# Optimization experiments

Hardware: AMD Instinct MI355X
Metric: run time of the kernel (lower is better)

Reference implementation:

```python
import jax, jax.numpy as jnp
import numpy as np
import math

DIM = 1024
N_HEADS = 16
HEAD_DIM = DIM // N_HEADS
FFN_HIDDEN = 4096
EPS = 1e-6


def setup_inputs() -> dict:
    key = jax.random.key(0)
    ks = jax.random.split(key, 10)
    s = 1.0 / math.sqrt(DIM)
    sh = 1.0 / math.sqrt(FFN_HIDDEN)
    return {
        "x": jax.random.normal(ks[0], (2, 2048, DIM), dtype=jnp.float32),
        # attention weights stored as [in, out] (y = x @ W)
        "wq": jax.random.normal(ks[1], (DIM, DIM), dtype=jnp.float32) * s,
        "wk": jax.random.normal(ks[2], (DIM, DIM), dtype=jnp.float32) * s,
        "wv": jax.random.normal(ks[3], (DIM, DIM), dtype=jnp.float32) * s,
        "wo": jax.random.normal(ks[4], (DIM, DIM), dtype=jnp.float32) * s,
        "w_gate": jax.random.normal(ks[5], (DIM, FFN_HIDDEN), dtype=jnp.float32) * s,
        "w_up": jax.random.normal(ks[6], (DIM, FFN_HIDDEN), dtype=jnp.float32) * s,
        "w_down": jax.random.normal(ks[7], (FFN_HIDDEN, DIM), dtype=jnp.float32) * sh,
        "attn_norm_w": jnp.ones((DIM,), dtype=jnp.float32),
        "ffn_norm_w": jnp.ones((DIM,), dtype=jnp.float32),
    }


def rmsnorm(x, w):
    xf = x.astype(jnp.float32)
    rms = jax.lax.rsqrt(jnp.mean(xf * xf, axis=-1, keepdims=True) + EPS)
    return (xf * rms).astype(x.dtype) * w


def attention(x, wq, wk, wv, wo):
    B, T, C = x.shape
    q = (x @ wq).reshape(B, T, N_HEADS, HEAD_DIM)
    k = (x @ wk).reshape(B, T, N_HEADS, HEAD_DIM)
    v = (x @ wv).reshape(B, T, N_HEADS, HEAD_DIM)
    scores = jnp.einsum("bqhd,bkhd->bhqk", q, k) / math.sqrt(HEAD_DIM)
    causal = jnp.tril(jnp.ones((T, T), dtype=bool))  # True = keep
    scores = jnp.where(causal, scores, -jnp.inf)
    attn = jax.nn.softmax(scores, axis=-1)
    out = jnp.einsum("bhqk,bkhd->bqhd", attn, v).reshape(B, T, C)
    return out @ wo


def swiglu(x, w_gate, w_up, w_down):
    return (jax.nn.silu(x @ w_gate) * (x @ w_up)) @ w_down


def reference(x, wq, wk, wv, wo, w_gate, w_up, w_down, attn_norm_w, ffn_norm_w):
    x = x + attention(rmsnorm(x, attn_norm_w), wq, wk, wv, wo)
    x = x + swiglu(rmsnorm(x, ffn_norm_w), w_gate, w_up, w_down)
    return x
```

## Files before the change

### kernel.cpp

```cpp
#include <hip/hip_runtime.h>
#include <hip/hip_bf16.h>
#include <stdint.h>
#include <math.h>

#define DIM   1024
#define TSEQ  2048
#define BATCH 2
#define NH    16
#define HD    64
#define FFN   4096
#define ROWS  (BATCH*TSEQ)
#define QKVN  (3*DIM)

typedef __attribute__((ext_vector_type(8))) short s16x8;
typedef __attribute__((ext_vector_type(4))) float f32x4;

__device__ __forceinline__ unsigned short f2bf(float f) {
  union { float f; unsigned u; } v; v.f = f;
  unsigned r = v.u + 0x7fffu + ((v.u >> 16) & 1u);
  return (unsigned short)(r >> 16);
}
__device__ __forceinline__ float bf2f(unsigned short h) {
  union { unsigned u; float f; } v; v.u = ((unsigned)h) << 16; return v.f;
}
__device__ __forceinline__ unsigned pack_bf2(float lo, float hi) {
  union { float f; unsigned u; } a, c; a.f = lo; c.f = hi;
  return (c.u & 0xffff0000u) | (a.u >> 16);
}

__device__ __forceinline__ void gld16(const void* g, void* l) {
  __builtin_amdgcn_global_load_lds((const __attribute__((address_space(1))) void*)g,
                                   (__attribute__((address_space(3))) void*)l, 16, 0, 0);
}

__device__ __forceinline__ int xcd_swz_flat() {
  const int nx = gridDim.x, ny = gridDim.y;
  const int nwg = nx * ny * gridDim.z;
  const int flat = blockIdx.x + nx * (blockIdx.y + ny * blockIdx.z);
  return (flat & 7) * (nwg >> 3) + (flat >> 3);
}

__global__ void wtrans_k(const float* __restrict__ w, unsigned short* __restrict__ wt,
                         int K, int N, int mode)
{
  __shared__ unsigned short t[64][65];
  const int n0 = blockIdx.x * 64, k0 = blockIdx.y * 64;
  const int tid = threadIdx.x;
  #pragma unroll
  for (int i = 0; i < 16; ++i) {
    const int r = i*4 + (tid >> 6), c = tid & 63;
    t[r][c] = f2bf(w[(size_t)(k0 + r) * N + n0 + c]);
  }
  __syncthreads();
  #pragma unroll
  for (int i = 0; i < 16; ++i) {
    const int r = i*4 + (tid >> 6), c = tid & 63;
    const int n = n0 + r;
    int dr = n;
    if (mode == 1) dr = ((n >> 4) << 5) + (n & 15);
    if (mode == 2) dr = ((n >> 4) << 5) + 16 + (n & 15);
    wt[(size_t)dr * K + k0 + c] = t[c][r];
  }
}

__global__ void wtrans_qkv_k(const float* __restrict__ wq, const float* __restrict__ wk,
                             const float* __restrict__ wv, unsigned short* __restrict__ wt)
{
  __shared__ unsigned short t[64][65];
  const int n0 = blockIdx.x * 64, k0 = blockIdx.y * 64, z = blockIdx.z;
  const float* w = (z == 0) ? wq : (z == 1) ? wk : wv;
  unsigned short* dst = wt + (size_t)z * DIM * DIM;
  const int tid = threadIdx.x;
  #pragma unroll
  for (int i = 0; i < 16; ++i) {
    const int r = i*4 + (tid >> 6), c = tid & 63;
    t[r][c] = f2bf(w[(size_t)(k0 + r) * DIM + n0 + c]);
  }
  __syncthreads();
  #pragma unroll
  for (int i = 0; i < 16; ++i) {
    const int r = i*4 + (tid >> 6), c = tid & 63;
    dst[(size_t)(n0 + r) * DIM + k0 + c] = t[c][r];
  }
}

__global__ void vtrans_k(const unsigned short* __restrict__ qkv, unsigned short* __restrict__ vt)
{
  __shared__ unsigned short t[64][65];
  const int tt0 = blockIdx.x * 64;
  const int bh = blockIdx.y, b = bh >> 4, h = bh & 15;
  const int tid = threadIdx.x;
  const unsigned short* src = qkv + (size_t)(b*TSEQ + tt0) * QKVN + 2*DIM + h*HD;
  #pragma unroll
  for (int i = 0; i < 16; ++i) {
    const int r = i*4 + (tid >> 6), c = tid & 63;
    t[r][c] = src[(size_t)r * QKVN + c];
  }
  __syncthreads();
  unsigned short* dst = vt + (size_t)bh * HD * TSEQ + tt0;
  #pragma unroll
  for (int i = 0; i < 16; ++i) {
    const int d = i*4 + (tid >> 6), c = tid & 63;
    dst[(size_t)d * TSEQ + c] = t[c][d];
  }
}

__global__ void rmsnorm_k(const float* __restrict__ x, const float* __restrict__ w,
                          unsigned short* __restrict__ o)
{
  const int row = blockIdx.x, tid = threadIdx.x;
  const float4 v = ((const float4*)(x + (size_t)row * DIM))[tid];
  float ss = v.x*v.x + v.y*v.y + v.z*v.z + v.w*v.w;
  #pragma unroll
  for (int off = 32; off >= 1; off >>= 1) ss += __shfl_xor(ss, off);
  __shared__ float sred[4];
  if ((tid & 63) == 0) sred[tid >> 6] = ss;
  __syncthreads();
  const float tot = sred[0] + sred[1] + sred[2] + sred[3];
  const float r = rsqrtf(tot * (1.0f/DIM) + 1e-6f);
  const float4 wv = ((const float4*)w)[tid];
  ushort4 ov;
  ov.x = f2bf(v.x*r*wv.x); ov.y = f2bf(v.y*r*wv.y);
  ov.z = f2bf(v.z*r*wv.z); ov.w = f2bf(v.w*r*wv.w);
  ((ushort4*)(o + (size_t)row * DIM))[tid] = ov;
}

__global__ void rmsnorm3_k(const float* __restrict__ x, const unsigned short* __restrict__ p0,
                           const unsigned short* __restrict__ p1, const float* __restrict__ w,
                           float* __restrict__ x1, unsigned short* __restrict__ o)
{
  const int row = blockIdx.x, tid = threadIdx.x;
  const size_t base = (size_t)row * DIM;
  const float4 a = ((const float4*)(x + base))[tid];
  const ushort4 b = ((const ushort4*)(p0 + base))[tid];
  const ushort4 c = ((const ushort4*)(p1 + base))[tid];
  float4 v;
  v.x = a.x + bf2f(b.x) + bf2f(c.x); v.y = a.y + bf2f(b.y) + bf2f(c.y);
  v.z = a.z + bf2f(b.z) + bf2f(c.z); v.w = a.w + bf2f(b.w) + bf2f(c.w);
  ((float4*)(x1 + base))[tid] = v;
  float ss = v.x*v.x + v.y*v.y + v.z*v.z + v.w*v.w;
  #pragma unroll
  for (int off = 32; off >= 1; off >>= 1) ss += __shfl_xor(ss, off);
  __shared__ float sred[4];
  if ((tid & 63) == 0) sred[tid >> 6] = ss;
  __syncthreads();
  const float tot = sred[0] + sred[1] + sred[2] + sred[3];
  const float r = rsqrtf(tot * (1.0f/DIM) + 1e-6f);
  const float4 wv = ((const float4*)w)[tid];
  ushort4 ov;
  ov.x = f2bf(v.x*r*wv.x); ov.y = f2bf(v.y*r*wv.y);
  ov.z = f2bf(v.z*r*wv.z); ov.w = f2bf(v.w*r*wv.w);
  ((ushort4*)(o + base))[tid] = ov;
}

__global__ void resadd5_k(const float* __restrict__ x1,
                          const unsigned short* __restrict__ q0, const unsigned short* __restrict__ q1,
                          const unsigned short* __restrict__ q2, const unsigned short* __restrict__ q3,
                          float* __restrict__ o)
{
  const size_t i = (size_t)blockIdx.x * 256 + threadIdx.x;
  const float4 a = ((const float4*)x1)[i];
  const ushort4 b = ((const ushort4*)q0)[i];
  const ushort4 c = ((const ushort4*)q1)[i];
  const ushort4 d = ((const ushort4*)q2)[i];
  const ushort4 e = ((const ushort4*)q3)[i];
  float4 v;
  v.x = a.x + bf2f(b.x) + bf2f(c.x) + bf2f(d.x) + bf2f(e.x);
  v.y = a.y + bf2f(b.y) + bf2f(c.y) + bf2f(d.y) + bf2f(e.y);
  v.z = a.z + bf2f(b.z) + bf2f(c.z) + bf2f(d.z) + bf2f(e.z);
  v.w = a.w + bf2f(b.w) + bf2f(c.w) + bf2f(d.w) + bf2f(e.w);
  ((float4*)o)[i] = v;
}

template<int NS>
__global__ void gemm128sp(const unsigned short* __restrict__ A, int lda,
                          const unsigned short* __restrict__ BT, int ldb,
                          unsigned short* __restrict__ P, int ldc, int Ksp)
{
  __shared__ __align__(16) unsigned short lA[128*64];
  __shared__ __align__(16) unsigned short lB[128*64];
  const int nx = gridDim.x, ny = gridDim.y;
  const int w = xcd_swz_flat();
  const int bx = w % nx, by = (w / nx) % ny, bz = w / (nx * ny);
  const int tid = threadIdx.x;
  const int lane = tid & 63;
  const int wid = tid >> 6;
  const int m0 = by * 128, n0 = bx * 128;
  const int Koff = bz * Ksp;
  P += (size_t)bz * ((size_t)ny * 128) * ldc;
  const int wr = (wid >> 1) * 64, wc = (wid & 1) * 64;
  const int lrow = lane & 15, lk8 = (lane >> 4) * 8;

  f32x4 acc[4][4] = {};

  for (int k0 = Koff; k0 < Koff + Ksp; k0 += 64) {
    #pragma unroll
    for (int c = 0; c < 4; ++c) {
      const int boff = c*4096 + tid*16;
      const int row = boff >> 7, colb = boff & 127;
      gld16((const char*)A + ((size_t)(m0+row)*lda + k0)*2 + colb, (char*)lA + boff);
    }
    #pragma unroll
    for (int c = 0; c < 4; ++c) {
      const int boff = c*4096 + tid*16;
      const int row = boff >> 7, colb = boff & 127;
      gld16((const char*)BT + ((size_t)(n0+row)*ldb + k0)*2 + colb, (char*)lB + boff);
    }
    __syncthreads();
    #pragma unroll
    for (int kk = 0; kk < 64; kk += 32) {
      s16x8 af[4], bf[4];
      #pragma unroll
      for (int i = 0; i < 4; ++i) af[i] = *(const s16x8*)&lA[(wr + i*16 + lrow)*64 + kk + lk8];
      #pragma unroll
      for (int j = 0; j < 4; ++j) bf[j] = *(const s16x8*)&lB[(wc + j*16 + lrow)*64 + kk + lk8];
      #pragma unroll
      for (int i = 0; i < 4; ++i)
        #pragma unroll
        for (int j = 0; j < 4; ++j)
          acc[i][j] = __builtin_amdgcn_mfma_f32_16x16x32_bf16(af[i], bf[j], acc[i][j], 0, 0, 0);
    }
    __syncthreads();
  }
  const int er = (lane >> 4) * 4, ec = lane & 15;
  #pragma unroll
  for (int i = 0; i < 4; ++i)
    #pragma unroll
    for (int j = 0; j < 4; ++j) {
      const int gr = m0 + wr + i*16 + er;
      const int gc = n0 + wc + j*16 + ec;
      #pragma unroll
      for (int e = 0; e < 4; ++e)
        P[(size_t)(gr + e) * ldc + gc] = f2bf(acc[i][j][e]);
    }
}

template<int EPI>
__global__ __launch_bounds__(512) void gemm256(const unsigned short* __restrict__ A, int lda,
                                               const unsigned short* __restrict__ BT, int ldb,
                                               void* __restrict__ Cout, int ldc, int K,
                                               int CX, int CY)
{
  __shared__ __align__(16) unsigned short lA[256*64];
  __shared__ __align__(16) unsigned short lB[256*64];
  const int nx = gridDim.x, ny = gridDim.y;
  const int flat = blockIdx.x + nx * blockIdx.y;
  const int xcd = flat & 7, kk_ = flat >> 3;
  const int RX = nx / CX, RY = ny / CY;
  const int cx = xcd % CX, cy = xcd / CX;
  const int bx = cx * RX + kk_ % RX;
  const int by = cy * RY + kk_ / RX;
  const int tid = threadIdx.x, lane = tid & 63, wid = tid >> 6;
  const int lrow = lane & 15, g = lane >> 4;
  const int wm = wid >> 2, wn = wid & 3;
  const int m0 = by * 256, n0 = bx * 256;

  const int r0 = tid >> 3;
  const int eB = ((r0 >> 5) << 6) | (r0 & 31);
  const int lc0 = ((tid & 7) * 16) ^ ((r0 & 7) << 4);
  const char* pA = (const char*)A + ((size_t)(m0 + r0) * lda) * 2 + lc0;
  const char* pB = (const char*)BT + ((size_t)(n0 + eB) * ldb) * 2 + lc0;
  char* dA = (char*)&lA[0] + tid * 16;
  char* dB = (char*)&lB[0] + eB * 128 + (tid & 7) * 16;
  const size_t a64 = (size_t)64 * lda * 2;
  const size_t b32 = (size_t)32 * ldb * 2;

#define STAGE(t) do { \
    const char* sa_ = pA + (size_t)(t) * 128; \
    gld16(sa_, dA);                 gld16(sa_ + 2*a64, dA + 16384); \
    gld16(sa_ + a64, dA + 8192);    gld16(sa_ + 3*a64, dA + 24576); \
    const char* sb_ = pB + (size_t)(t) * 128; \
    gld16(sb_, dB);                 gld16(sb_ + 4*b32, dB + 16384); \
    gld16(sb_ + b32, dB + 4096);    gld16(sb_ + 5*b32, dB + 20480); \
  } while (0)

  const int swz = (lrow & 7) << 4;
  const int c0 = (g * 16) ^ swz;
  const int c1 = c0 ^ 64;
  const char* rdA = (const char*)&lA[0] + (wm * 128 + lrow) * 128;
  const char* rdB = (const char*)&lB[0] + (wn * 64 + lrow) * 128;

  f32x4 acc[8][4] = {};
  s16x8 a0[4][2], a1[4][2], b0[2][2], b1[2][2];

#define MFMA_Q(rh, ch, AF, BF) do { \
    _Pragma("unroll") \
    for (int i_ = 0; i_ < 4; ++i_) { \
      _Pragma("unroll") \
      for (int j_ = 0; j_ < 2; ++j_) { \
        acc[(rh)*4+i_][(ch)*2+j_] = __builtin_amdgcn_mfma_f32_16x16x32_bf16(AF[i_][0], BF[j_][0], acc[(rh)*4+i_][(ch)*2+j_], 0,0,0); \
        acc[(rh)*4+i_][(ch)*2+j_] = __builtin_amdgcn_mfma_f32_16x16x32_bf16(AF[i_][1], BF[j_][1], acc[(rh)*4+i_][(ch)*2+j_], 0,0,0); \
      } } } while (0)

#define VMCNT(n) asm volatile("s_waitcnt vmcnt(" #n ")" ::: "memory")
#define LGKM(n)  do { asm volatile("s_waitcnt lgkmcnt(" #n ")" ::: "memory"); \
                      __builtin_amdgcn_sched_barrier(0); } while (0)
#define BARRIER() do { __builtin_amdgcn_s_barrier(); \
                       __builtin_amdgcn_sched_barrier(0); } while (0)

#define RD_A0() do { _Pragma("unroll") for (int i_ = 0; i_ < 4; ++i_) { \
    a0[i_][0] = *(const s16x8*)(rdA + i_*2048 + c0); \
    a0[i_][1] = *(const s16x8*)(rdA + i_*2048 + c1); } } while (0)
#define RD_A1() do { _Pragma("unroll") for (int i_ = 0; i_ < 4; ++i_) { \
    a1[i_][0] = *(const s16x8*)(rdA + 8192 + i_*2048 + c0); \
    a1[i_][1] = *(const s16x8*)(rdA + 8192 + i_*2048 + c1); } } while (0)
#define RD_B0() do { _Pragma("unroll") for (int j_ = 0; j_ < 2; ++j_) { \
    b0[j_][0] = *(const s16x8*)(rdB + j_*2048 + c0); \
    b0[j_][1] = *(const s16x8*)(rdB + j_*2048 + c1); } } while (0)
#define RD_B1() do { _Pragma("unroll") for (int j_ = 0; j_ < 2; ++j_) { \
    b1[j_][0] = *(const s16x8*)(rdB + 4096 + j_*2048 + c0); \
    b1[j_][1] = *(const s16x8*)(rdB + 4096 + j_*2048 + c1); } } while (0)

  const int NT = K >> 6;

  STAGE(0);

  for (int t = 0; t < NT; ++t) {
    VMCNT(0);
    BARRIER();
    RD_A0(); RD_B0(); RD_B1();
    LGKM(4);
    __builtin_amdgcn_s_setprio(1);
    MFMA_Q(0, 0, a0, b0);
    __builtin_amdgcn_s_setprio(0);
    LGKM(0);
    __builtin_amdgcn_s_setprio(1);
    MFMA_Q(0, 1, a0, b1);
    __builtin_amdgcn_s_setprio(0);
    RD_A1();
    LGKM(0);
    __builtin_amdgcn_s_setprio(1);
    MFMA_Q(1, 0, a1, b0);
    MFMA_Q(1, 1, a1, b1);
    __builtin_amdgcn_s_setprio(0);
    BARRIER();
    if (t + 1 < NT) STAGE(t + 1);
  }

  const int er = g * 4, ec = lane & 15;
  if (EPI == 0) {
    unsigned short* C = (unsigned short*)Cout;
    #pragma unroll
    for (int i = 0; i < 8; ++i)
      #pragma unroll
      for (int j = 0; j < 4; ++j) {
        const int gr = m0 + wm*128 + i*16 + er;
        const int gc = n0 + wn*64 + j*16 + ec;
        #pragma unroll
        for (int e = 0; e < 4; ++e)
          C[(size_t)(gr + e) * ldc + gc] = f2bf(acc[i][j][e]);
      }
  } else {
    unsigned short* C = (unsigned short*)Cout;
    #pragma unroll
    for (int i = 0; i < 8; ++i)
      #pragma unroll
      for (int tp = 0; tp < 2; ++tp) {
        const int gr = m0 + wm*128 + i*16 + er;
        const int hc = (n0 >> 1) + wn*32 + tp*16 + ec;
        #pragma unroll
        for (int e = 0; e < 4; ++e) {
          const float gv = acc[i][2*tp][e];
          const float uv = acc[i][2*tp + 1][e];
          const float hv = gv / (1.f + __expf(-gv)) * uv;
          C[(size_t)(gr + e) * ldc + hc] = f2bf(hv);
        }
      }
  }
#undef STAGE
#undef MFMA_Q
#undef VMCNT
#undef LGKM
#undef BARRIER
#undef RD_A0
#undef RD_A1
#undef RD_B0
#undef RD_B1
}

__global__ __launch_bounds__(512) void attn_fwd(const unsigned short* __restrict__ qkv,
                                                const unsigned short* __restrict__ vt,
                                                unsigned short* __restrict__ outp)
{
  __shared__ __align__(16) unsigned short lK[2][64*64];
  __shared__ __align__(16) unsigned short lV[2][64*64];
  const int nx = gridDim.x;
  const int wsz = xcd_swz_flat();
  const int qblk = wsz % nx;
  const int bh = wsz / nx, b = bh >> 4, h = bh & 15;
  const int tid = threadIdx.x, wid = tid >> 6, lane = tid & 63;
  const int lq = lane & 15, g = lane >> 4;

  const int qrow = qblk*128 + wid*16;
  const int myq = qrow + lq;

  const size_t qbase = ((size_t)(b*TSEQ + myq)) * QKVN + h*HD;
  const s16x8 qf0 = *(const s16x8*)&qkv[qbase + g*8];
  const s16x8 qf1 = *(const s16x8*)&qkv[qbase + 32 + g*8];

  const int boff = tid * 16;
  const int loff = boff ^ (((boff >> 7) & 7) << 4);
  const int srow = loff >> 7;
  const int scolb = loff & 127;
  const char* ksrc0 = (const char*)qkv +
      (((size_t)(b*TSEQ + srow)) * QKVN + DIM + h*HD) * 2 + scolb;
  const char* vsrc0 = (const char*)vt +
      (((size_t)bh*HD + srow) * TSEQ) * 2 + scolb;

  float mrun = -INFINITY, lrun = 0.f;
  f32x4 of[4] = {};

  const int nkt = 2*qblk + 2;

  gld16(ksrc0, (char*)lK[0] + boff);
  gld16(vsrc0, (char*)lV[0] + boff);
  int cur = 0;

  for (int kt = 0; kt < nkt; ++kt) {
    __syncthreads();
    if (kt + 1 < nkt) {
      gld16(ksrc0 + (size_t)(kt+1)*64*(QKVN*2), (char*)lK[cur^1] + boff);
      gld16(vsrc0 + (size_t)(kt+1)*128,         (char*)lV[cur^1] + boff);
    }
    if (kt*64 <= qrow + 15) {
      const unsigned short* Kb = lK[cur];
      const unsigned short* Vb = lV[cur];
      f32x4 sacc[4] = {};
      #pragma unroll
      for (int s = 0; s < 4; ++s) {
        const int r = s*16 + lq;
        const int sw = (r & 7) << 4;
        const s16x8 kf0 = *(const s16x8*)((const char*)Kb + r*128 + ((g*16) ^ sw));
        const s16x8 kf1 = *(const s16x8*)((const char*)Kb + r*128 + ((64 + g*16) ^ sw));
        sacc[s] = __builtin_amdgcn_mfma_f32_16x16x32_bf16(kf0, qf0, sacc[s], 0,0,0);
        sacc[s] = __builtin_amdgcn_mfma_f32_16x16x32_bf16(kf1, qf1, sacc[s], 0,0,0);
      }
      float p[4][4];
      float mt = -INFINITY;
      #pragma unroll
      for (int s = 0; s < 4; ++s)
        #pragma unroll
        for (int e = 0; e < 4; ++e) {
          const int key = kt*64 + s*16 + 4*g + e;
          const float v = (key <= myq) ? sacc[s][e]*0.125f : -INFINITY;
          p[s][e] = v;
          mt = fmaxf(mt, v);
        }
      mt = fmaxf(mt, __shfl_xor(mt, 16));
      mt = fmaxf(mt, __shfl_xor(mt, 32));
      const float mnew = fmaxf(mrun, mt);
      const float scale = __expf(mrun - mnew);
      float ssum = 0.f;
      #pragma unroll
      for (int s = 0; s < 4; ++s)
        #pragma unroll
        for (int e = 0; e < 4; ++e) {
          p[s][e] = __expf(p[s][e] - mnew);
          ssum += p[s][e];
        }
      ssum += __shfl_xor(ssum, 16);
      ssum += __shfl_xor(ssum, 32);
      lrun = lrun * scale + ssum;
      mrun = mnew;
      #pragma unroll
      for (int d0b = 0; d0b < 4; ++d0b) of[d0b] = of[d0b] * scale;
      #pragma unroll
      for (int hh = 0; hh < 2; ++hh) {
        unsigned w[4];
        #pragma unroll
        for (int j = 0; j < 4; ++j) w[j] = pack_bf2(p[2*hh][j], p[2*hh+1][j]);
        s16x8 bp;
        #pragma unroll
        for (int e = 0; e < 8; ++e) {
          const int srcg = 2*(g & 1) + (e >> 2);
          const unsigned ww = (unsigned)__shfl((int)w[e & 3], lq | (srcg << 4));
          bp[e] = (short)((g >= 2) ? (ww >> 16) : (ww & 0xffffu));
        }
        #pragma unroll
        for (int d0b = 0; d0b < 4; ++d0b) {
          const int r = d0b*16 + lq;
          const int sw = (r & 7) << 4;
          const s16x8 vf = *(const s16x8*)((const char*)Vb + r*128 + ((hh*64 + g*16) ^ sw));
          of[d0b] = __builtin_amdgcn_mfma_f32_16x16x32_bf16(vf, bp, of[d0b], 0,0,0);
        }
      }
    }
    cur ^= 1;
  }
  const float inv = 1.f / lrun;
  const size_t obase = ((size_t)(b*TSEQ + myq)) * DIM + h*HD;
  #pragma unroll
  for (int d0b = 0; d0b < 4; ++d0b) {
    ushort4 o;
    o.x = f2bf(of[d0b][0] * inv);
    o.y = f2bf(of[d0b][1] * inv);
    o.z = f2bf(of[d0b][2] * inv);
    o.w = f2bf(of[d0b][3] * inv);
    *(ushort4*)&outp[obase + d0b*16 + 4*g] = o;
  }
}

extern "C" void kernel_launch(void* const* d_in, const int* in_sizes, int n_in,
                              void* d_out, int out_size, void* d_ws, size_t ws_size,
                              hipStream_t stream)
{
  const float* x   = (const float*)d_in[0];
  const float* wq  = (const float*)d_in[1];
  const float* wk  = (const float*)d_in[2];
  const float* wv  = (const float*)d_in[3];
  const float* wo  = (const float*)d_in[4];
  const float* wg  = (const float*)d_in[5];
  const float* wu  = (const float*)d_in[6];
  const float* wd  = (const float*)d_in[7];
  const float* anw = (const float*)d_in[8];
  const float* fnw = (const float*)d_in[9];
  float* outp = (float*)d_out;

  const size_t MB = 1024*1024;
  const size_t RD = (size_t)ROWS * DIM;
  char* ws = (char*)d_ws;
  float*          x1    = (float*)         (ws + 0);
  unsigned short* wdT   = (unsigned short*)(ws + 16*MB);
  unsigned short* wguT  = (unsigned short*)(ws + 24*MB);
  unsigned short* wqkvT = (unsigned short*)(ws + 40*MB);
  unsigned short* woT   = (unsigned short*)(ws + 46*MB);
  unsigned short* xn    = (unsigned short*)(ws + 48*MB);
  unsigned short* qkv   = (unsigned short*)(ws + 56*MB);
  unsigned short* vtb   = (unsigned short*)(ws + 80*MB);
  unsigned short* aout  = (unsigned short*)(ws + 88*MB);
  unsigned short* pwo   = (unsigned short*)(ws + 56*MB);
  unsigned short* hbuf  = (unsigned short*)(ws + 56*MB);
  unsigned short* pdn   = (unsigned short*)(ws + 24*MB);

  const dim3 blk(256);

  wtrans_qkv_k<<<dim3(16,16,3), blk, 0, stream>>>(wq, wk, wv, wqkvT);
  wtrans_k<<<dim3(16,16), blk, 0, stream>>>(wo, woT, DIM, DIM, 0);
  wtrans_k<<<dim3(64,16), blk, 0, stream>>>(wg, wguT, DIM, FFN, 1);
  wtrans_k<<<dim3(64,16), blk, 0, stream>>>(wu, wguT, DIM, FFN, 2);
  wtrans_k<<<dim3(16,64), blk, 0, stream>>>(wd, wdT, FFN, DIM, 0);

  rmsnorm_k<<<ROWS, blk, 0, stream>>>(x, anw, xn);
  gemm256<0><<<dim3(QKVN/256, ROWS/256), dim3(512), 0, stream>>>(xn, DIM, wqkvT, DIM, qkv, QKVN, DIM, 4, 2);
  vtrans_k<<<dim3(TSEQ/64, BATCH*NH), blk, 0, stream>>>(qkv, vtb);
  attn_fwd<<<dim3(TSEQ/128, BATCH*NH), dim3(512), 0, stream>>>(qkv, vtb, aout);
  gemm128sp<2><<<dim3(DIM/128, ROWS/128, 2), blk, 0, stream>>>(aout, DIM, woT, DIM, pwo, DIM, DIM/2);
  rmsnorm3_k<<<ROWS, blk, 0, stream>>>(x, pwo, pwo + RD, fnw, x1, xn);

  gemm256<2><<<dim3(2*FFN/256, ROWS/256), dim3(512), 0, stream>>>(xn, DIM, wguT, DIM, hbuf, FFN, DIM, 4, 2);
  gemm128sp<4><<<dim3(DIM/128, ROWS/128, 4), blk, 0, stream>>>(hbuf, FFN, wdT, FFN, pdn, DIM, FFN/4);
  resadd5_k<<<dim3(ROWS*DIM/1024), blk, 0, stream>>>(x1, pdn, pdn + RD, pdn + 2*RD, pdn + 3*RD, outp);
}
```

Measured before the change: 312.0 us.

## Shrink gemm256 tile to 256x128 with K=32 double-buffered LDS pipeline

```diff
diff --git a/kernel.cpp b/kernel.cpp
--- a/kernel.cpp
+++ b/kernel.cpp
@@ -236,13 +236,13 @@
 }
 
 template<int EPI>
-__global__ __launch_bounds__(512) void gemm256(const unsigned short* __restrict__ A, int lda,
-                                               const unsigned short* __restrict__ BT, int ldb,
-                                               void* __restrict__ Cout, int ldc, int K,
-                                               int CX, int CY)
-{
-  __shared__ __align__(16) unsigned short lA[256*64];
-  __shared__ __align__(16) unsigned short lB[256*64];
+__global__ __launch_bounds__(512, 4) void gemm256(const unsigned short* __restrict__ A, int lda,
+                                                  const unsigned short* __restrict__ BT, int ldb,
+                                                  void* __restrict__ Cout, int ldc, int K,
+                                                  int CX, int CY)
+{
+  __shared__ __align__(16) unsigned short lA[2][256*32];
+  __shared__ __align__(16) unsigned short lB[2][128*32];
   const int nx = gridDim.x, ny = gridDim.y;
   const int flat = blockIdx.x + nx * blockIdx.y;
   const int xcd = flat & 7, kk_ = flat >> 3;
@@ -252,99 +252,73 @@
   const int by = cy * RY + kk_ / RX;
   const int tid = threadIdx.x, lane = tid & 63, wid = tid >> 6;
   const int lrow = lane & 15, g = lane >> 4;
-  const int wm = wid >> 2, wn = wid & 3;
-  const int m0 = by * 256, n0 = bx * 256;
-
-  const int r0 = tid >> 3;
-  const int eB = ((r0 >> 5) << 6) | (r0 & 31);
-  const int lc0 = ((tid & 7) * 16) ^ ((r0 & 7) << 4);
-  const char* pA = (const char*)A + ((size_t)(m0 + r0) * lda) * 2 + lc0;
-  const char* pB = (const char*)BT + ((size_t)(n0 + eB) * ldb) * 2 + lc0;
-  char* dA = (char*)&lA[0] + tid * 16;
-  char* dB = (char*)&lB[0] + eB * 128 + (tid & 7) * 16;
-  const size_t a64 = (size_t)64 * lda * 2;
-  const size_t b32 = (size_t)32 * ldb * 2;
+  const int wm = wid >> 1, wn = wid & 1;
+  const int m0 = by * 256, n0 = bx * 128;
+
+  const int pa = tid * 16;
+  const int La = pa ^ (((pa >> 7) & 7) << 4);
+  const int ra = La >> 6, kba = La & 63;
+  const int Lb = La;
+  const int rb = Lb >> 6, kbb = Lb & 63;
+  const char* pA1 = (const char*)A + ((size_t)(m0 + ra) * lda) * 2 + kba;
+  const char* pA2 = (const char*)A + ((size_t)(m0 + ra + 128) * lda) * 2 + kba;
+  const char* pB1 = (const char*)BT + ((size_t)(n0 + rb) * ldb) * 2 + kbb;
 
 #define STAGE(t) do { \
-    const char* sa_ = pA + (size_t)(t) * 128; \
-    gld16(sa_, dA);                 gld16(sa_ + 2*a64, dA + 16384); \
-    gld16(sa_ + a64, dA + 8192);    gld16(sa_ + 3*a64, dA + 24576); \
-    const char* sb_ = pB + (size_t)(t) * 128; \
-    gld16(sb_, dB);                 gld16(sb_ + 4*b32, dB + 16384); \
-    gld16(sb_ + b32, dB + 4096);    gld16(sb_ + 5*b32, dB + 20480); \
+    char* dA_ = (char*)&lA[(t) & 1][0] + pa; \
+    char* dB_ = (char*)&lB[(t) & 1][0] + pa; \
+    const size_t kof_ = (size_t)(t) * 64; \
+    gld16(pA1 + kof_, dA_); \
+    gld16(pA2 + kof_, dA_ + 8192); \
+    gld16(pB1 + kof_, dB_); \
   } while (0)
 
-  const int swz = (lrow & 7) << 4;
-  const int c0 = (g * 16) ^ swz;
-  const int c1 = c0 ^ 64;
-  const char* rdA = (const char*)&lA[0] + (wm * 128 + lrow) * 128;
-  const char* rdB = (const char*)&lB[0] + (wn * 64 + lrow) * 128;
-
-  f32x4 acc[8][4] = {};
-  s16x8 a0[4][2], a1[4][2], b0[2][2], b1[2][2];
-
-#define MFMA_Q(rh, ch, AF, BF) do { \
-    _Pragma("unroll") \
-    for (int i_ = 0; i_ < 4; ++i_) { \
-      _Pragma("unroll") \
-      for (int j_ = 0; j_ < 2; ++j_) { \
-        acc[(rh)*4+i_][(ch)*2+j_] = __builtin_amdgcn_mfma_f32_16x16x32_bf16(AF[i_][0], BF[j_][0], acc[(rh)*4+i_][(ch)*2+j_], 0,0,0); \
-        acc[(rh)*4+i_][(ch)*2+j_] = __builtin_amdgcn_mfma_f32_16x16x32_bf16(AF[i_][1], BF[j_][1], acc[(rh)*4+i_][(ch)*2+j_], 0,0,0); \
-      } } } while (0)
-
-#define VMCNT(n) asm volatile("s_waitcnt vmcnt(" #n ")" ::: "memory")
-#define LGKM(n)  do { asm volatile("s_waitcnt lgkmcnt(" #n ")" ::: "memory"); \
+  const int aoff = (lrow * 64 + g * 16) ^ (((lrow >> 1) & 7) << 4);
+
+  f32x4 acc[4][4] = {};
+  s16x8 af[4], bf[4];
+
+#define LGKM0()  do { asm volatile("s_waitcnt lgkmcnt(0)" ::: "memory"); \
                       __builtin_amdgcn_sched_barrier(0); } while (0)
+#define VMCNT0() asm volatile("s_waitcnt vmcnt(0)" ::: "memory")
 #define BARRIER() do { __builtin_amdgcn_s_barrier(); \
                        __builtin_amdgcn_sched_barrier(0); } while (0)
 
-#define RD_A0() do { _Pragma("unroll") for (int i_ = 0; i_ < 4; ++i_) { \
-    a0[i_][0] = *(const s16x8*)(rdA + i_*2048 + c0); \
-    a0[i_][1] = *(const s16x8*)(rdA + i_*2048 + c1); } } while (0)
-#define RD_A1() do { _Pragma("unroll") for (int i_ = 0; i_ < 4; ++i_) { \
-    a1[i_][0] = *(const s16x8*)(rdA + 8192 + i_*2048 + c0); \
-    a1[i_][1] = *(const s16x8*)(rdA + 8192 + i_*2048 + c1); } } while (0)
-#define RD_B0() do { _Pragma("unroll") for (int j_ = 0; j_ < 2; ++j_) { \
-    b0[j_][0] = *(const s16x8*)(rdB + j_*2048 + c0); \
-    b0[j_][1] = *(const s16x8*)(rdB + j_*2048 + c1); } } while (0)
-#define RD_B1() do { _Pragma("unroll") for (int j_ = 0; j_ < 2; ++j_) { \
-    b1[j_][0] = *(const s16x8*)(rdB + 4096 + j_*2048 + c0); \
-    b1[j_][1] = *(const s16x8*)(rdB + 4096 + j_*2048 + c1); } } while (0)
-
-  const int NT = K >> 6;
+  const int NT = K >> 5;
 
   STAGE(0);
+  VMCNT0();
+  BARRIER();
 
   for (int t = 0; t < NT; ++t) {
-    VMCNT(0);
+    if (t + 1 < NT) STAGE(t + 1);
+    const char* bufA = (const char*)&lA[t & 1][0] + wm * 4096;
+    const char* bufB = (const char*)&lB[t & 1][0] + wn * 4096;
+    #pragma unroll
+    for (int i = 0; i < 4; ++i) af[i] = *(const s16x8*)(bufA + i*1024 + aoff);
+    #pragma unroll
+    for (int j = 0; j < 4; ++j) bf[j] = *(const s16x8*)(bufB + j*1024 + aoff);
     BARRIER();
-    RD_A0(); RD_B0(); RD_B1();
-    LGKM(4);
+    LGKM0();
     __builtin_amdgcn_s_setprio(1);
-    MFMA_Q(0, 0, a0, b0);
+    #pragma unroll
+    for (int i = 0; i < 4; ++i)
+      #pragma unroll
+      for (int j = 0; j < 4; ++j)
+        acc[i][j] = __builtin_amdgcn_mfma_f32_16x16x32_bf16(af[i], bf[j], acc[i][j], 0, 0, 0);
     __builtin_amdgcn_s_setprio(0);
-    LGKM(0);
-    __builtin_amdgcn_s_setprio(1);
-    MFMA_Q(0, 1, a0, b1);
-    __builtin_amdgcn_s_setprio(0);
-    RD_A1();
-    LGKM(0);
-    __builtin_amdgcn_s_setprio(1);
-    MFMA_Q(1, 0, a1, b0);
-    MFMA_Q(1, 1, a1, b1);
-    __builtin_amdgcn_s_setprio(0);
+    VMCNT0();
     BARRIER();
-    if (t + 1 < NT) STAGE(t + 1);
   }
 
   const int er = g * 4, ec = lane & 15;
   if (EPI == 0) {
     unsigned short* C = (unsigned short*)Cout;
     #pragma unroll
-    for (int i = 0; i < 8; ++i)
+    for (int i = 0; i < 4; ++i)
       #pragma unroll
       for (int j = 0; j < 4; ++j) {
-        const int gr = m0 + wm*128 + i*16 + er;
+        const int gr = m0 + wm*64 + i*16 + er;
         const int gc = n0 + wn*64 + j*16 + ec;
         #pragma unroll
         for (int e = 0; e < 4; ++e)
@@ -353,10 +327,10 @@
   } else {
     unsigned short* C = (unsigned short*)Cout;
     #pragma unroll
-    for (int i = 0; i < 8; ++i)
+    for (int i = 0; i < 4; ++i)
       #pragma unroll
       for (int tp = 0; tp < 2; ++tp) {
-        const int gr = m0 + wm*128 + i*16 + er;
+        const int gr = m0 + wm*64 + i*16 + er;
         const int hc = (n0 >> 1) + wn*32 + tp*16 + ec;
         #pragma unroll
         for (int e = 0; e < 4; ++e) {
@@ -368,14 +342,9 @@
       }
   }
 #undef STAGE
-#undef MFMA_Q
-#undef VMCNT
-#undef LGKM
+#undef LGKM0
+#undef VMCNT0
 #undef BARRIER
-#undef RD_A0
-#undef RD_A1
-#undef RD_B0
-#undef RD_B1
 }
 
 __global__ __launch_bounds__(512) void attn_fwd(const unsigned short* __restrict__ qkv,
@@ -541,13 +510,13 @@
   wtrans_k<<<dim3(16,64), blk, 0, stream>>>(wd, wdT, FFN, DIM, 0);
 
   rmsnorm_k<<<ROWS, blk, 0, stream>>>(x, anw, xn);
-  gemm256<0><<<dim3(QKVN/256, ROWS/256), dim3(512), 0, stream>>>(xn, DIM, wqkvT, DIM, qkv, QKVN, DIM, 4, 2);
+  gemm256<0><<<dim3(QKVN/128, ROWS/256), dim3(512), 0, stream>>>(xn, DIM, wqkvT, DIM, qkv, QKVN, DIM, 4, 2);
   vtrans_k<<<dim3(TSEQ/64, BATCH*NH), blk, 0, stream>>>(qkv, vtb);
   attn_fwd<<<dim3(TSEQ/128, BATCH*NH), dim3(512), 0, stream>>>(qkv, vtb, aout);
   gemm128sp<2><<<dim3(DIM/128, ROWS/128, 2), blk, 0, stream>>>(aout, DIM, woT, DIM, pwo, DIM, DIM/2);
   rmsnorm3_k<<<ROWS, blk, 0, stream>>>(x, pwo, pwo + RD, fnw, x1, xn);
 
-  gemm256<2><<<dim3(2*FFN/256, ROWS/256), dim3(512), 0, stream>>>(xn, DIM, wguT, DIM, hbuf, FFN, DIM, 4, 2);
+  gemm256<2><<<dim3(2*FFN/128, ROWS/256), dim3(512), 0, stream>>>(xn, DIM, wguT, DIM, hbuf, FFN, DIM, 4, 2);
   gemm128sp<4><<<dim3(DIM/128, ROWS/128, 4), blk, 0, stream>>>(hbuf, FFN, wdT, FFN, pdn, DIM, FFN/4);
   resadd5_k<<<dim3(ROWS*DIM/1024), blk, 0, stream>>>(x1, pdn, pdn + RD, pdn + 2*RD, pdn + 3*RD, outp);
 }
```

After: 306.5 us. No clear change (-1.8%).
